# Kernel optimization log

Hardware: AMD Instinct MI355X
Metric: run time of the kernel (lower is better)

The kernel has to match this reference:

```python
import jax, jax.numpy as jnp
import numpy as np

DEPTH, IN_DIM, GRID, HID, BATCH = 3, 256, 64, 128, 4096
BN_EPS = 1e-5

def _lin(key, fi, fo):
    kw, kb = jax.random.split(key)
    bound = 1.0 / np.sqrt(fi)
    w = jax.random.uniform(kw, (fi, fo), jnp.float32, -bound, bound)
    b = jax.random.uniform(kb, (fo,), jnp.float32, -bound, bound)
    return w, b

def setup_inputs() -> dict:
    key = jax.random.key(0)
    ks = jax.random.split(key, 8)
    x = jax.random.normal(ks[0], (BATCH, IN_DIM), jnp.float32)
    fs = jax.random.normal(ks[1], (DEPTH, IN_DIM, GRID, HID), jnp.float32)
    grids = jnp.tile(jnp.linspace(0.0, 1.0, GRID, dtype=jnp.float32)[None, :], (DEPTH, 1))
    w1, b1 = _lin(ks[2], HID, HID * 2)
    w2, b2 = _lin(ks[3], HID * 2, HID)
    w3, b3 = _lin(ks[4], HID, HID // 2)
    w4, b4 = _lin(ks[5], HID // 2, 1)
    return {
        "x": x, "fs": fs, "grids": grids,
        "w1": w1, "b1": b1, "g1": jnp.ones(HID * 2), "be1": jnp.zeros(HID * 2),
        "w2": w2, "b2": b2, "g2": jnp.ones(HID), "be2": jnp.zeros(HID),
        "w3": w3, "b3": b3, "g3": jnp.ones(HID // 2), "be3": jnp.zeros(HID // 2),
        "w4": w4, "b4": b4,
    }

def _bn(a, g, b):
    # BatchNorm1d, training mode: biased batch variance, eps=1e-5
    m = a.mean(0)
    v = a.var(0)
    return (a - m) / jnp.sqrt(v + BN_EPS) * g + b

def reference(x, fs, grids, w1, b1, g1, be1, w2, b2, g2, be2, w3, b3, g3, be3, w4, b4):
    # per-feature min-max normalization over the batch
    zmin = x.min(0)
    zmax = x.max(0)
    z = (x - zmin) / (zmax - zmin + 1e-6)  # (B, I)
    h = jnp.zeros((x.shape[0], fs.shape[-1]), x.dtype)
    for i in range(fs.shape[0]):  # small fixed depth
        Bm = jax.nn.relu(z[:, :, None] - grids[i][None, None, :])  # (B, I, G)
        # fused multiply-reduce over grid AND input dims: (b,i,g) x (i,g,h) -> (b,h)
        h = h + jnp.einsum('big,igh->bh', Bm, fs[i])
    a = _bn(jax.nn.relu(h @ w1 + b1), g1, be1)
    a = _bn(jax.nn.relu(a @ w2 + b2), g2, be2)
    a = _bn(jax.nn.relu(a @ w3 + b3), g3, be3)
    return a @ w4 + b4  # (B, 1)
```

## Files before the change

### kernel.cpp

```cpp
#include <hip/hip_runtime.h>
#include <hip/hip_fp16.h>

#define BATCH 4096
#define IN_DIM 256
#define GRID_N 64
#define HID 128
#define GEMM_GB 256
#define PCHUNKS 16
constexpr float BN_EPS = 1e-5f;

typedef _Float16 h2 __attribute__((ext_vector_type(2)));
__device__ __forceinline__ h2 as_h2(unsigned u){ union {unsigned x; h2 h;} c; c.x = u; return c.h; }

static const size_t O_MMP  = 0;
static const size_t O_P1   = 32768;
static const size_t O_P2   = O_P1 + 524288;
static const size_t O_P3   = O_P2 + 262144;
static const size_t O_PI1  = O_P3 + 131072;
static const size_t O_PI2  = O_PI1 + 32768;
static const size_t O_STB  = O_PI2 + 16384;
static const size_t O_A1   = O_STB + (size_t)256*65*128*4;
static const size_t O_A2   = O_A1 + (size_t)4096*256*4;
static const size_t O_A3   = O_A2 + (size_t)4096*128*4;
static const size_t O_H    = O_A3 + (size_t)4096*64*4;

__global__ __launch_bounds__(256) void k_prep(const float* __restrict__ x, const float* __restrict__ fs,
                                              const float* __restrict__ grids,
                                              float* __restrict__ mmp, unsigned* __restrict__ STb){
    const int tid = threadIdx.x;
    const int bid = blockIdx.x;
    if (bid < 16){
        const float* xp = x + (size_t)bid*256*IN_DIM + tid;
        float mn = 1e30f, mx = -1e30f;
        #pragma unroll 8
        for (int r = 0; r < 256; ++r){
            float v = xp[(size_t)r*IN_DIM];
            mn = fminf(mn, v); mx = fmaxf(mx, v);
        }
        mmp[(size_t)bid*512 + tid]       = mn;
        mmp[(size_t)bid*512 + 256 + tid] = mx;
        return;
    }
    const int i = (bid - 16)*2 + (tid >> 7);
    const int h = tid & 127;
    const float* f0 = fs + ((size_t)(0*IN_DIM + i)*GRID_N)*HID + h;
    const float* f1 = fs + ((size_t)(1*IN_DIM + i)*GRID_N)*HID + h;
    const float* f2 = fs + ((size_t)(2*IN_DIM + i)*GRID_N)*HID + h;
    unsigned* st = STb + (size_t)i*65*HID + h;
    float acc1 = 0.f, acc2 = 0.f;
    st[0] = 0u;
    #pragma unroll 4
    for (int k = 0; k < 64; ++k){
        float fv = f0[(size_t)k*HID] + f1[(size_t)k*HID] + f2[(size_t)k*HID];
        float g  = grids[k];
        acc1 += fv;
        acc2  = fmaf(g, fv, acc2);
        __half2 hh = __halves2half2(__float2half_rn(acc1), __float2half_rn(-acc2));
        st[(size_t)(k+1)*HID] = *reinterpret_cast<unsigned*>(&hh);
    }
}

__global__ __launch_bounds__(128) void k_gather(const float* __restrict__ x, const float* __restrict__ mmp,
                                                const unsigned* __restrict__ STb, float* __restrict__ h){
    __shared__ float s_zmin[256], s_inv[256];
    __shared__ uint2 pre[2][256];
    const int tid = threadIdx.x;
    const int b0  = blockIdx.x * 2;

    for (int f = tid; f < 256; f += 128){
        float mn = 1e30f, mx = -1e30f;
        #pragma unroll
        for (int p = 0; p < 16; ++p){
            mn = fminf(mn, mmp[(size_t)p*512 + f]);
            mx = fmaxf(mx, mmp[(size_t)p*512 + 256 + f]);
        }
        s_zmin[f] = mn;
        s_inv[f]  = 1.0f / (mx - mn + 1e-6f);
    }
    __syncthreads();

    for (int idx = tid; idx < 2*256; idx += 128){
        int bl = idx >> 8, i = idx & 255;
        float z = (x[(size_t)(b0 + bl)*IN_DIM + i] - s_zmin[i]) * s_inv[i];
        int K0 = (int)(z * 63.0f) + 1;
        K0 = max(1, min(63, K0));
        unsigned off = ((unsigned)(i*65 + K0)) << 9;
        __half2 zh = __halves2half2(__float2half_rn(z), __float2half_rn(1.0f));
        pre[bl][i] = make_uint2(*reinterpret_cast<unsigned*>(&zh), off);
    }
    __syncthreads();

    const int w  = tid >> 6;
    const int l  = tid & 63;
    const int hl = l & 31;
    const int hi = l >> 5;
    const char* base = (const char*)STb + (size_t)hl * 16;
    const uint2* pp = &pre[w][hi * 128];
    float acc0 = 0.f, acc1 = 0.f, acc2 = 0.f, acc3 = 0.f;
    #pragma unroll 8
    for (int ii = 0; ii < 128; ++ii){
        uint2 p = pp[ii];
        uint4 u = *reinterpret_cast<const uint4*>(base + p.y);
        h2 zz = as_h2(p.x);
        acc0 = __builtin_amdgcn_fdot2(zz, as_h2(u.x), acc0, false);
        acc1 = __builtin_amdgcn_fdot2(zz, as_h2(u.y), acc1, false);
        acc2 = __builtin_amdgcn_fdot2(zz, as_h2(u.z), acc2, false);
        acc3 = __builtin_amdgcn_fdot2(zz, as_h2(u.w), acc3, false);
    }
    acc0 += __shfl(acc0, hl + 32);
    acc1 += __shfl(acc1, hl + 32);
    acc2 += __shfl(acc2, hl + 32);
    acc3 += __shfl(acc3, hl + 32);
    if (hi == 0){
        *reinterpret_cast<float4*>(&h[(size_t)(b0 + w)*HID + 4*hl]) =
            make_float4(acc0, acc1, acc2, acc3);
    }
}

__global__ __launch_bounds__(256) void k_stats(const float* __restrict__ part, float* __restrict__ pint,
                                               int twoN){
    int j = blockIdx.x*256 + threadIdx.x;
    if (j >= twoN) return;
    const int p0 = blockIdx.y * (GEMM_GB/PCHUNKS);
    float s = 0.f;
    #pragma unroll
    for (int p = 0; p < GEMM_GB/PCHUNKS; ++p) s += part[(size_t)(p0 + p)*twoN + j];
    pint[(size_t)blockIdx.y*twoN + j] = s;
}

template<int BN_IN>
__global__ __launch_bounds__(256) void k_gemm(const float* __restrict__ A, const float* __restrict__ W,
                                              const float* __restrict__ bias,
                                              const float* __restrict__ pint,
                                              const float* __restrict__ gam, const float* __restrict__ bet,
                                              float* __restrict__ C, float* __restrict__ outpart,
                                              int K, int N){
    __shared__ float As[16][64];
    __shared__ float Ws[64][64];
    __shared__ float bnsc[256], bnsh[256];
    __shared__ float red[16][16][8];

    const int tid = threadIdx.x;
    const int n0  = blockIdx.x * 64;
    const int b0  = blockIdx.y * 16;

    if (BN_IN){
        for (int k = tid; k < K; k += 256){
            float s = 0.f, ss = 0.f;
            #pragma unroll
            for (int r = 0; r < PCHUNKS; ++r){
                s  += pint[(size_t)r*(2*K) + k];
                ss += pint[(size_t)r*(2*K) + K + k];
            }
            float m  = s  * (1.0f/BATCH);
            float v  = ss * (1.0f/BATCH) - m*m;
            float rs = rsqrtf(v + BN_EPS);
            float sc = gam[k]*rs;
            bnsc[k] = sc;
            bnsh[k] = fmaf(-m, sc, bet[k]);
        }
        __syncthreads();
    }

    const int nt = tid & 15;
    const int bt = tid >> 4;
    float acc[4] = {0.f, 0.f, 0.f, 0.f};

    for (int kc = 0; kc < K; kc += 64){
        #pragma unroll
        for (int idx = tid; idx < 16*64; idx += 256){
            int r = idx >> 6, k = idx & 63;
            float a = A[(size_t)(b0 + r)*K + kc + k];
            if (BN_IN) a = fmaf(a, bnsc[kc + k], bnsh[kc + k]);
            As[r][k] = a;
        }
        #pragma unroll
        for (int idx = tid; idx < 64*64; idx += 256){
            int k = idx >> 6, n = idx & 63;
            Ws[k][n] = W[(size_t)(kc + k)*N + n0 + n];
        }
        __syncthreads();
        #pragma unroll
        for (int k = 0; k < 64; ++k){
            float4 w = *reinterpret_cast<const float4*>(&Ws[k][nt*4]);
            float a0 = As[bt][k];
            acc[0] = fmaf(a0, w.x, acc[0]); acc[1] = fmaf(a0, w.y, acc[1]);
            acc[2] = fmaf(a0, w.z, acc[2]); acc[3] = fmaf(a0, w.w, acc[3]);
        }
        __syncthreads();
    }

    float vv[4];
    #pragma unroll
    for (int j = 0; j < 4; ++j){
        float v1 = acc[j] + bias[n0 + nt*4 + j];
        vv[j] = fmaxf(v1, 0.f);
    }
    *reinterpret_cast<float4*>(&C[(size_t)(b0 + bt)*N + n0 + nt*4]) =
        make_float4(vv[0], vv[1], vv[2], vv[3]);
    #pragma unroll
    for (int j = 0; j < 4; ++j){
        red[bt][nt][j]   = vv[j];
        red[bt][nt][4+j] = vv[j]*vv[j];
    }
    __syncthreads();
    for (int s = 8; s > 0; s >>= 1){
        if (bt < s){
            #pragma unroll
            for (int f = 0; f < 8; ++f) red[bt][nt][f] += red[bt+s][nt][f];
        }
        __syncthreads();
    }
    if (bt == 0){
        float* op = outpart + (size_t)blockIdx.y*(2*N);
        #pragma unroll
        for (int j = 0; j < 4; ++j){
            op[n0 + nt*4 + j]     = red[0][nt][j];
            op[N + n0 + nt*4 + j] = red[0][nt][4+j];
        }
    }
}

__global__ __launch_bounds__(256) void k_final(const float* __restrict__ A3, const float* __restrict__ p3,
                                               const float* __restrict__ g3, const float* __restrict__ be3,
                                               const float* __restrict__ w4, const float* __restrict__ b4,
                                               float* __restrict__ out){
    __shared__ float psum[2][128];
    __shared__ float sc[64], sh[64];
    const int t = threadIdx.x;
    {
        int j = t & 127, half = t >> 7;
        float s = 0.f;
        #pragma unroll 8
        for (int p = half*128; p < half*128 + 128; ++p) s += p3[(size_t)p*128 + j];
        psum[half][j] = s;
    }
    __syncthreads();
    if (t < 64){
        float s  = psum[0][t]      + psum[1][t];
        float ss = psum[0][64 + t] + psum[1][64 + t];
        float m  = s  * (1.0f/BATCH);
        float v  = ss * (1.0f/BATCH) - m*m;
        float rs = rsqrtf(v + BN_EPS);
        float g  = g3[t]*rs;
        sc[t] = g * w4[t];
        sh[t] = fmaf(-m, g, be3[t]) * w4[t];
    }
    __syncthreads();
    int row = blockIdx.x*256 + t;
    const float* a = A3 + (size_t)row*64;
    float acc = b4[0];
    #pragma unroll
    for (int k = 0; k < 64; ++k){
        acc = fmaf(a[k], sc[k], acc);
        acc += sh[k];
    }
    out[row] = acc;
}

extern "C" void kernel_launch(void* const* d_in, const int* in_sizes, int n_in,
                              void* d_out, int out_size, void* d_ws, size_t ws_size,
                              hipStream_t stream){
    const float* x     = (const float*)d_in[0];
    const float* fs    = (const float*)d_in[1];
    const float* grids = (const float*)d_in[2];
    const float* w1 = (const float*)d_in[3];  const float* b1 = (const float*)d_in[4];
    const float* g1 = (const float*)d_in[5];  const float* be1= (const float*)d_in[6];
    const float* w2 = (const float*)d_in[7];  const float* b2 = (const float*)d_in[8];
    const float* g2 = (const float*)d_in[9];  const float* be2= (const float*)d_in[10];
    const float* w3 = (const float*)d_in[11]; const float* b3 = (const float*)d_in[12];
    const float* g3 = (const float*)d_in[13]; const float* be3= (const float*)d_in[14];
    const float* w4 = (const float*)d_in[15]; const float* b4 = (const float*)d_in[16];
    float* out = (float*)d_out;

    char* ws = (char*)d_ws;
    float* mmp    = (float*)(ws + O_MMP);
    float* p1     = (float*)(ws + O_P1);
    float* p2     = (float*)(ws + O_P2);
    float* p3     = (float*)(ws + O_P3);
    float* pi1    = (float*)(ws + O_PI1);
    float* pi2    = (float*)(ws + O_PI2);
    unsigned* STb = (unsigned*)(ws + O_STB);
    float* A1     = (float*)(ws + O_A1);
    float* A2     = (float*)(ws + O_A2);
    float* A3     = (float*)(ws + O_A3);
    float* h      = (float*)(ws + O_H);

    k_prep<<<144, 256, 0, stream>>>(x, fs, grids, mmp, STb);
    k_gather<<<2048, 128, 0, stream>>>(x, mmp, STb, h);
    k_gemm<0><<<dim3(4, 256), 256, 0, stream>>>(h,  w1, b1, nullptr, nullptr, nullptr, A1, p1, 128, 256);
    k_stats<<<dim3(2, PCHUNKS), 256, 0, stream>>>(p1, pi1, 512);
    k_gemm<1><<<dim3(2, 256), 256, 0, stream>>>(A1, w2, b2, pi1, g1, be1, A2, p2, 256, 128);
    k_stats<<<dim3(1, PCHUNKS), 256, 0, stream>>>(p2, pi2, 256);
    k_gemm<1><<<dim3(1, 256), 256, 0, stream>>>(A2, w3, b3, pi2, g2, be2, A3, p3, 128, 64);
    k_final<<<16, 256, 0, stream>>>(A3, p3, g3, be3, w4, b4, out);
}
```

Measured before the change: 102.8 us.

## Split prefix-sum over grid into two halves per feature with shared-memory carry

The fs prefix-sum pass in k_prep now gives each input feature its own block. Two thread halves each scan 32 grid points, and the second half adds the first half's carry through shared memory. This doubles the number of prep blocks from 128 to 256 and halves the serial dependent chain of loads per thread, aiming to expose more memory parallelism when reading the 25 MB fs tensor. It costs extra registers for the 64 buffered partial sums and adds a block-level barrier.

```diff
diff --git a/kernel.cpp b/kernel.cpp
--- a/kernel.cpp
+++ b/kernel.cpp
@@ -41,22 +41,42 @@
         mmp[(size_t)bid*512 + 256 + tid] = mx;
         return;
     }
-    const int i = (bid - 16)*2 + (tid >> 7);
-    const int h = tid & 127;
-    const float* f0 = fs + ((size_t)(0*IN_DIM + i)*GRID_N)*HID + h;
-    const float* f1 = fs + ((size_t)(1*IN_DIM + i)*GRID_N)*HID + h;
-    const float* f2 = fs + ((size_t)(2*IN_DIM + i)*GRID_N)*HID + h;
+    __shared__ float carry1[128], carry2[128];
+    const int i  = bid - 16;
+    const int h  = tid & 127;
+    const int kh = tid >> 7;
+    const int kb = kh * 32;
+    const float* f0 = fs + ((size_t)(0*IN_DIM + i)*GRID_N + kb)*HID + h;
+    const float* f1 = fs + ((size_t)(1*IN_DIM + i)*GRID_N + kb)*HID + h;
+    const float* f2 = fs + ((size_t)(2*IN_DIM + i)*GRID_N + kb)*HID + h;
     unsigned* st = STb + (size_t)i*65*HID + h;
     float acc1 = 0.f, acc2 = 0.f;
-    st[0] = 0u;
-    #pragma unroll 4
-    for (int k = 0; k < 64; ++k){
+    float l1[32], l2[32];
+    #pragma unroll
+    for (int k = 0; k < 32; ++k){
         float fv = f0[(size_t)k*HID] + f1[(size_t)k*HID] + f2[(size_t)k*HID];
-        float g  = grids[k];
+        float g  = grids[kb + k];
         acc1 += fv;
         acc2  = fmaf(g, fv, acc2);
-        __half2 hh = __halves2half2(__float2half_rn(acc1), __float2half_rn(-acc2));
-        st[(size_t)(k+1)*HID] = *reinterpret_cast<unsigned*>(&hh);
+        l1[k] = acc1; l2[k] = acc2;
+    }
+    if (kh == 0){
+        st[0] = 0u;
+        carry1[h] = acc1; carry2[h] = acc2;
+        #pragma unroll
+        for (int k = 0; k < 32; ++k){
+            __half2 hh = __halves2half2(__float2half_rn(l1[k]), __float2half_rn(-l2[k]));
+            st[(size_t)(k+1)*HID] = *reinterpret_cast<unsigned*>(&hh);
+        }
+    }
+    __syncthreads();
+    if (kh == 1){
+        float c1 = carry1[h], c2 = carry2[h];
+        #pragma unroll
+        for (int k = 0; k < 32; ++k){
+            __half2 hh = __halves2half2(__float2half_rn(l1[k] + c1), __float2half_rn(-(l2[k] + c2)));
+            st[(size_t)(33 + k)*HID] = *reinterpret_cast<unsigned*>(&hh);
+        }
     }
 }
 
@@ -286,7 +306,7 @@
     float* A3     = (float*)(ws + O_A3);
     float* h      = (float*)(ws + O_H);
 
-    k_prep<<<144, 256, 0, stream>>>(x, fs, grids, mmp, STb);
+    k_prep<<<272, 256, 0, stream>>>(x, fs, grids, mmp, STb);
     k_gather<<<2048, 128, 0, stream>>>(x, mmp, STb, h);
     k_gemm<0><<<dim3(4, 256), 256, 0, stream>>>(h,  w1, b1, nullptr, nullptr, nullptr, A1, p1, 128, 256);
     k_stats<<<dim3(2, PCHUNKS), 256, 0, stream>>>(p1, pi1, 512);
```

After: 103.0 us. About the same (+0.1%).
